# Kernel optimization log

Hardware: AMD Instinct MI355X
Metric: run time of the kernel (lower is better)

Reference implementation:

```python
import jax, jax.numpy as jnp
import numpy as np

N = 100000   # nodes
E = 1200000  # edges
D = 64       # input_features == hidden_features
L = 3        # num_layers
EPS = 1e-5   # BatchNorm1d eps
SLOPE = 0.2  # LeakyReLU negative slope


def setup_inputs() -> dict:
    key = jax.random.key(0)
    k_x, k_e, k_w = jax.random.split(key, 3)
    x = jax.random.normal(k_x, (N, D), dtype=jnp.float32)
    edge_index = jax.random.randint(k_e, (2, E), 0, N, dtype=jnp.int32)
    # Glorot-ish linear weights per layer, stacked [L, D, D]; bias zeros.
    Ws = jax.random.normal(k_w, (L, D, D), dtype=jnp.float32) / np.float32(np.sqrt(D))
    bs = jnp.zeros((L, D), dtype=jnp.float32)
    # BatchNorm affine params (training-mode batch statistics are used).
    gammas = jnp.ones((L, D), dtype=jnp.float32)
    betas = jnp.zeros((L, D), dtype=jnp.float32)
    return {"x": x, "edge_index": edge_index, "Ws": Ws, "bs": bs,
            "gammas": gammas, "betas": betas}


def reference(x, edge_index, Ws, bs, gammas, betas):
    src, dst = edge_index[0], edge_index[1]
    # GCN symmetric normalization with self-loops: deg = in-degree + 1
    deg = jax.ops.segment_sum(jnp.ones((E,), x.dtype), dst, num_segments=N) + 1.0
    dinv = jax.lax.rsqrt(deg)
    enorm = (dinv[src] * dinv[dst])[:, None]  # [E,1] edge norm
    snorm = (dinv * dinv)[:, None]            # [N,1] self-loop norm
    for l in range(L):
        xw = x @ Ws[l]                                        # [N,D]
        agg = (jax.ops.segment_sum(xw[src] * enorm, dst, num_segments=N)
               + xw * snorm + bs[l])                          # GCNConv output
        h = jnp.where(agg > 0, agg, SLOPE * agg)              # LeakyReLU(0.2)
        mu = h.mean(axis=0)
        var = h.var(axis=0)                                   # biased var (PyTorch BN)
        x = gammas[l] * (h - mu) * jax.lax.rsqrt(var + EPS) + betas[l]
    return x
```

## Files before the change

### kernel.cpp

```cpp
#include <hip/hip_runtime.h>

#define D 64
#define SLOPE 0.2f
#define BN_EPS 1e-5f
#define BSHIFT 9
#define BUCKET 512
#define CHUNK 8192
#define CAP 7168
#define COLCAP (CAP + 7 * BUCKET)

static __device__ __forceinline__ unsigned pk_bf16(float fx, float fy) {
    unsigned bx = __float_as_uint(fx);
    unsigned by = __float_as_uint(fy);
    bx = (bx + 0x7fffu + ((bx >> 16) & 1u)) >> 16;
    by = (by + 0x7fffu + ((by >> 16) & 1u)) & 0xffff0000u;
    return bx | by;
}
static __device__ __forceinline__ float bf_lo(unsigned u) { return __uint_as_float(u << 16); }
static __device__ __forceinline__ float bf_hi(unsigned u) { return __uint_as_float(u & 0xffff0000u); }

__global__ __launch_bounds__(256) void k_part(const int* __restrict__ src,
                                              const int* __restrict__ dst,
                                              int* __restrict__ pcur,
                                              unsigned* __restrict__ arena, int E) {
    __shared__ unsigned stage[CHUNK];
    __shared__ unsigned char bktb[CHUNK];
    __shared__ int hist[256], lofs[256], gbase[256];
    const int t = threadIdx.x;
    const int e0 = blockIdx.x * CHUNK;
    const int cn = min(CHUNK, E - e0);

    hist[t] = 0;
    __syncthreads();
    for (int i = t; i < cn; i += 256)
        atomicAdd(&hist[dst[e0 + i] >> BSHIFT], 1);
    __syncthreads();
    const int v = hist[t];
    lofs[t] = v;
    __syncthreads();
    for (int off = 1; off < 256; off <<= 1) {
        int x = lofs[t];
        if (t >= off) x += lofs[t - off];
        __syncthreads();
        lofs[t] = x;
        __syncthreads();
    }
    const int excl = lofs[t] - v;
    __syncthreads();
    lofs[t] = excl;
    if (v > 0) gbase[t] = t * CAP + atomicAdd(&pcur[t], v);
    __syncthreads();
    for (int i = t; i < cn; i += 256) {
        const int dd = dst[e0 + i];
        const int b  = dd >> BSHIFT;
        const int p  = atomicAdd(&lofs[b], 1);
        stage[p] = ((unsigned)(dd & (BUCKET - 1)) << 23) | (unsigned)src[e0 + i];
        bktb[p]  = (unsigned char)b;
    }
    __syncthreads();
    for (int i = t; i < cn; i += 256) {
        const int b = bktb[i];
        const int startb = lofs[b] - hist[b];
        arena[gbase[b] + (i - startb)] = stage[i];
    }
}

__global__ __launch_bounds__(512) void k_build(const unsigned* __restrict__ arena,
                                               const int* __restrict__ pcur,
                                               int* __restrict__ rp, int* __restrict__ pcnt,
                                               int* __restrict__ colbuf, float* __restrict__ dinv,
                                               unsigned* __restrict__ ybf, int N, int HS) {
    __shared__ int ncnt[512], sc[512], lcur[512];
    const int t = threadIdx.x;
    const int b = blockIdx.x;
    const int nbase  = b << BSHIFT;
    const int nlocal = min(BUCKET, N - nbase);
    const int count  = pcur[b];
    const unsigned* ab = arena + (size_t)b * CAP;
    const int colbase = b * COLCAP;

    if (b == 0 && t < 32)
        ybf[(size_t)(t >> 4) * HS + (size_t)N * 16 + (t & 15)] = 0u;

    ncnt[t] = 0;
    __syncthreads();
    for (int i = t; i < count; i += 512)
        atomicAdd(&ncnt[ab[i] >> 23], 1);
    __syncthreads();
    const int v = ncnt[t];
    const int p = (v + 7) & ~7;
    sc[t] = p;
    __syncthreads();
    for (int off = 1; off < 512; off <<= 1) {
        int x = sc[t];
        if (t >= off) x += sc[t - off];
        __syncthreads();
        sc[t] = x;
        __syncthreads();
    }
    const int excl = sc[t] - p;
    lcur[t] = colbase + excl;
    if (t < nlocal) {
        rp[nbase + t]   = colbase + excl;
        pcnt[nbase + t] = p;
        dinv[nbase + t] = rsqrtf((float)v + 1.0f);
    }
    __syncthreads();
    for (int i = t; i < count; i += 512) {
        const unsigned u = ab[i];
        const int pos = atomicAdd(&lcur[u >> 23], 1);
        colbuf[pos] = (int)(u & 0x7FFFFFu);
    }
    if (t < nlocal)
        for (int k = v; k < p; ++k) colbuf[colbase + excl + k] = N;
}

__global__ __launch_bounds__(256) void k_gemm(const float* __restrict__ x,
                                              const float* __restrict__ W,
                                              const float* __restrict__ stats,
                                              const float* __restrict__ gamma,
                                              const float* __restrict__ beta,
                                              const float* __restrict__ dinv,
                                              unsigned* __restrict__ ybf,
                                              float invN, int affine, int N, int HS) {
    __shared__ float scs[D], shs[D];
    const int tid = threadIdx.x;
    if (tid < D) {
        float sc = 1.f, sh = 0.f;
        if (affine) {
            const float mu  = stats[tid] * invN;
            const float var = stats[D + tid] * invN - mu * mu;
            sc = gamma[tid] * rsqrtf(var + BN_EPS);
            sh = beta[tid] - mu * sc;
        }
        scs[tid] = sc; shs[tid] = sh;
    }
    __syncthreads();
    const int lane = tid & 63;
    const int wib  = tid >> 6;
    const int half = lane >> 5;
    const int sl16 = (lane >> 1) & 15;
    float Wreg[D];
    float bv = 0.f;
#pragma unroll
    for (int k = 0; k < D; ++k) {
        const float w = W[k * D + lane];
        Wreg[k] = scs[k] * w;
        bv = fmaf(shs[k], w, bv);
    }
    const int stride = gridDim.x * 4;
    for (int row = __builtin_amdgcn_readfirstlane(blockIdx.x * 4 + wib); row < N; row += stride) {
        const float4* xr = (const float4*)(x + (size_t)row * D);
        float acc = 0.f;
#pragma unroll
        for (int k4 = 0; k4 < 16; ++k4) {
            const float4 xv = xr[k4];
            acc = fmaf(xv.x, Wreg[4 * k4 + 0], acc);
            acc = fmaf(xv.y, Wreg[4 * k4 + 1], acc);
            acc = fmaf(xv.z, Wreg[4 * k4 + 2], acc);
            acc = fmaf(xv.w, Wreg[4 * k4 + 3], acc);
        }
        const float r  = (acc + bv) * dinv[row];
        const float rn = __shfl_down(r, 1, 64);
        if (!(lane & 1))
            ybf[(size_t)half * HS + (size_t)row * 16 + sl16] = pk_bf16(r, rn);
    }
}

__global__ __launch_bounds__(256) void k_pull(const int* __restrict__ rp,
                                              const int* __restrict__ pcnt,
                                              const int* __restrict__ colbuf,
                                              const unsigned* __restrict__ ybf,
                                              const float* __restrict__ dinv,
                                              const float* __restrict__ b,
                                              float* __restrict__ h,
                                              float* __restrict__ stats, int N, int HS) {
    const int tid  = threadIdx.x;
    const int lane = tid & 63;
    const int t16  = lane & 15;
    const int qw   = lane >> 4;
    const int wv   = tid >> 6;
    const int gw   = blockIdx.x * 4 + wv;
    const int gstride = gridDim.x * 4;

    float s1[2][2] = {{0.f, 0.f}, {0.f, 0.f}};
    float s2[2][2] = {{0.f, 0.f}, {0.f, 0.f}};

#pragma unroll
    for (int half = 0; half < 2; ++half) {
        const unsigned* yb = ybf + (size_t)half * HS;
        const float b0 = b[half * 32 + 2 * t16];
        const float b1 = b[half * 32 + 2 * t16 + 1];

        for (int pr = gw; 4 * pr < N; pr += gstride) {
            const int n  = 4 * pr + qw;
            const bool vn = n < N;
            const int st = vn ? rp[n]   : 0;
            const int pd = vn ? pcnt[n] : 0;

            float a[8][2];
#pragma unroll
            for (int c = 0; c < 8; ++c) { a[c][0] = 0.f; a[c][1] = 0.f; }
            {
                const unsigned u = vn ? yb[(size_t)n * 16 + t16] : 0u;
                a[0][0] = bf_lo(u); a[0][1] = bf_hi(u);
            }
            for (int w0 = 0; w0 < pd; w0 += 16) {
                const int wn = min(pd - w0, 16);
                const int ci = (t16 < wn) ? colbuf[st + w0 + t16] : 0;
                for (int j0 = 0; j0 < wn; j0 += 8) {
#pragma unroll
                    for (int jj = 0; jj < 8; ++jj) {
                        const int idx = __shfl(ci, qw * 16 + j0 + jj, 64);
                        const unsigned u = yb[(size_t)idx * 16 + t16];
                        a[jj][0] += bf_lo(u);
                        a[jj][1] += bf_hi(u);
                    }
                }
            }
            const float v0 = ((a[0][0] + a[1][0]) + (a[2][0] + a[3][0])) +
                             ((a[4][0] + a[5][0]) + (a[6][0] + a[7][0]));
            const float v1 = ((a[0][1] + a[1][1]) + (a[2][1] + a[3][1])) +
                             ((a[4][1] + a[5][1]) + (a[6][1] + a[7][1]));
            if (vn) {
                const float di = dinv[n];
                float t0 = fmaf(di, v0, b0); t0 = t0 > 0.f ? t0 : SLOPE * t0;
                float t1 = fmaf(di, v1, b1); t1 = t1 > 0.f ? t1 : SLOPE * t1;
                *(float2*)&h[(size_t)n * D + half * 32 + 2 * t16] = make_float2(t0, t1);
                s1[half][0] += t0; s2[half][0] += t0 * t0;
                s1[half][1] += t1; s2[half][1] += t1 * t1;
            }
        }
    }

    __shared__ float l1[64], l2[64];
    if (tid < 64) { l1[tid] = 0.f; l2[tid] = 0.f; }
    __syncthreads();
#pragma unroll
    for (int half = 0; half < 2; ++half) {
        atomicAdd(&l1[half * 32 + 2 * t16],     s1[half][0]);
        atomicAdd(&l1[half * 32 + 2 * t16 + 1], s1[half][1]);
        atomicAdd(&l2[half * 32 + 2 * t16],     s2[half][0]);
        atomicAdd(&l2[half * 32 + 2 * t16 + 1], s2[half][1]);
    }
    __syncthreads();
    if (tid < 64) {
        atomicAdd(&stats[tid],      l1[tid]);
        atomicAdd(&stats[64 + tid], l2[tid]);
    }
}

__global__ __launch_bounds__(256) void k_normalize(const float* __restrict__ h,
                                                   const float* __restrict__ stats,
                                                   const float* __restrict__ gamma,
                                                   const float* __restrict__ beta,
                                                   float* __restrict__ out,
                                                   float invN, int total4) {
    const int gt = blockIdx.x * 256 + threadIdx.x;
    const int c0 = (gt * 4) & 63;
    float sc[4], sh[4];
#pragma unroll
    for (int k = 0; k < 4; ++k) {
        const int c = c0 + k;
        const float mu  = stats[c] * invN;
        const float var = stats[64 + c] * invN - mu * mu;
        sc[k] = gamma[c] * rsqrtf(var + BN_EPS);
        sh[k] = beta[c] - mu * sc[k];
    }
    const float4* h4 = (const float4*)h;
    float4* o4 = (float4*)out;
    for (int i = gt; i < total4; i += gridDim.x * 256) {
        float4 v = h4[i];
        v.x = fmaf(sc[0], v.x, sh[0]);
        v.y = fmaf(sc[1], v.y, sh[1]);
        v.z = fmaf(sc[2], v.z, sh[2]);
        v.w = fmaf(sc[3], v.w, sh[3]);
        o4[i] = v;
    }
}

extern "C" void kernel_launch(void* const* d_in, const int* in_sizes, int n_in,
                              void* d_out, int out_size, void* d_ws, size_t ws_size,
                              hipStream_t stream) {
    const float* x0     = (const float*)d_in[0];
    const int*   ei     = (const int*)d_in[1];
    const float* Ws     = (const float*)d_in[2];
    const float* bs     = (const float*)d_in[3];
    const float* gammas = (const float*)d_in[4];
    const float* betas  = (const float*)d_in[5];

    const int N = in_sizes[0] / D;
    const int E = in_sizes[1] / 2;
    const int L = in_sizes[2] / (D * D);
    const int nchunks = (E + CHUNK - 1) / CHUNK;
    const int NB = (N + BUCKET - 1) >> BSHIFT;
    const int HS = (N + 1) * 16;

    const int* srcp = ei;
    const int* dstp = ei + E;

    char* wsb = (char*)d_ws;
    size_t o = 0;
    auto alloc = [&](size_t elems) { size_t r = o; o += (elems + 255) & ~(size_t)255; return r; };
    const size_t o_pcur  = alloc(256);
    const size_t o_stats = alloc((size_t)L * 128);
    const size_t zero_end = o;
    const size_t o_rp    = alloc((size_t)N);
    const size_t o_pcnt  = alloc((size_t)N);
    const size_t o_dinv  = alloc((size_t)N);
    const size_t o_arena = alloc((size_t)NB * CAP);
    const size_t o_col   = alloc((size_t)NB * COLCAP);
    const size_t o_y     = alloc((size_t)2 * HS);

    int*      pcur  = (int*)(wsb + o_pcur * 4);
    float*    stats = (float*)(wsb + o_stats * 4);
    int*      rp    = (int*)(wsb + o_rp * 4);
    int*      pcnt  = (int*)(wsb + o_pcnt * 4);
    float*    dinv  = (float*)(wsb + o_dinv * 4);
    unsigned* arena = (unsigned*)(wsb + o_arena * 4);
    int*      col   = (int*)(wsb + o_col * 4);
    unsigned* ybf   = (unsigned*)(wsb + o_y * 4);
    float*    out   = (float*)d_out;
    float*    h     = out;

    hipMemsetAsync(d_ws, 0, zero_end * 4, stream);

    k_part <<<nchunks, 256, 0, stream>>>(srcp, dstp, pcur, arena, E);
    k_build<<<NB, 512, 0, stream>>>(arena, pcur, rp, pcnt, col, dinv, ybf, N, HS);

    const float invN = 1.0f / (float)N;
    const float* xin = x0;
    for (int l = 0; l < L; ++l) {
        const int pl = l ? l - 1 : 0;
        k_gemm<<<1024, 256, 0, stream>>>(xin, Ws + (size_t)l * D * D,
                                         stats + (size_t)pl * 128,
                                         gammas + (size_t)pl * D, betas + (size_t)pl * D,
                                         dinv, ybf, invN, l > 0 ? 1 : 0, N, HS);
        k_pull<<<2048, 256, 0, stream>>>(rp, pcnt, col, ybf, dinv,
                                         bs + (size_t)l * D, h,
                                         stats + (size_t)l * 128, N, HS);
        xin = h;
    }
    k_normalize<<<1024, 256, 0, stream>>>(h, stats + (size_t)(L - 1) * 128,
                                          gammas + (size_t)(L - 1) * D,
                                          betas + (size_t)(L - 1) * D,
                                          out, invN, N * D / 4);
}
```

Baseline: 442.5 us.

## Store bf16 features as full 128-byte rows and gather in one pass

Replaces the split layout, where each node's 64 bf16 features sat in two separate 64-byte half-planes gathered in two passes, with a single interleaved layout of 128 bytes per node. The pull kernel now handles two nodes per wavefront with 32 lanes each and gathers every neighbor row once, which halves the colbuf index reads and loop passes. The cost is a larger per-row gather footprint, which may reduce L2 hit locality compared with the half-plane scheme. Per-lane degree imbalance now spans two nodes instead of four.

```diff
diff --git a/kernel.cpp b/kernel.cpp
--- a/kernel.cpp
+++ b/kernel.cpp
@@ -69,7 +69,7 @@
                                                const int* __restrict__ pcur,
                                                int* __restrict__ rp, int* __restrict__ pcnt,
                                                int* __restrict__ colbuf, float* __restrict__ dinv,
-                                               unsigned* __restrict__ ybf, int N, int HS) {
+                                               unsigned* __restrict__ ybf, int N) {
     __shared__ int ncnt[512], sc[512], lcur[512];
     const int t = threadIdx.x;
     const int b = blockIdx.x;
@@ -79,8 +79,7 @@
     const unsigned* ab = arena + (size_t)b * CAP;
     const int colbase = b * COLCAP;
 
-    if (b == 0 && t < 32)
-        ybf[(size_t)(t >> 4) * HS + (size_t)N * 16 + (t & 15)] = 0u;
+    if (b == 0 && t < 32) ybf[(size_t)N * 32 + t] = 0u;
 
     ncnt[t] = 0;
     __syncthreads();
@@ -122,7 +121,7 @@
                                               const float* __restrict__ beta,
                                               const float* __restrict__ dinv,
                                               unsigned* __restrict__ ybf,
-                                              float invN, int affine, int N, int HS) {
+                                              float invN, int affine, int N) {
     __shared__ float scs[D], shs[D];
     const int tid = threadIdx.x;
     if (tid < D) {
@@ -138,8 +137,6 @@
     __syncthreads();
     const int lane = tid & 63;
     const int wib  = tid >> 6;
-    const int half = lane >> 5;
-    const int sl16 = (lane >> 1) & 15;
     float Wreg[D];
     float bv = 0.f;
 #pragma unroll
@@ -163,7 +160,7 @@
         const float r  = (acc + bv) * dinv[row];
         const float rn = __shfl_down(r, 1, 64);
         if (!(lane & 1))
-            ybf[(size_t)half * HS + (size_t)row * 16 + sl16] = pk_bf16(r, rn);
+            ybf[(size_t)row * 32 + (lane >> 1)] = pk_bf16(r, rn);
     }
 }
 
@@ -174,75 +171,65 @@
                                               const float* __restrict__ dinv,
                                               const float* __restrict__ b,
                                               float* __restrict__ h,
-                                              float* __restrict__ stats, int N, int HS) {
+                                              float* __restrict__ stats, int N) {
     const int tid  = threadIdx.x;
     const int lane = tid & 63;
-    const int t16  = lane & 15;
-    const int qw   = lane >> 4;
+    const int t32  = lane & 31;
+    const int hw   = lane >> 5;
     const int wv   = tid >> 6;
-    const int gw   = blockIdx.x * 4 + wv;
+    const float b0 = b[2 * t32];
+    const float b1 = b[2 * t32 + 1];
+    float s1a = 0.f, s1b = 0.f, s2a = 0.f, s2b = 0.f;
+    const int gw = blockIdx.x * 4 + wv;
     const int gstride = gridDim.x * 4;
 
-    float s1[2][2] = {{0.f, 0.f}, {0.f, 0.f}};
-    float s2[2][2] = {{0.f, 0.f}, {0.f, 0.f}};
-
-#pragma unroll
-    for (int half = 0; half < 2; ++half) {
-        const unsigned* yb = ybf + (size_t)half * HS;
-        const float b0 = b[half * 32 + 2 * t16];
-        const float b1 = b[half * 32 + 2 * t16 + 1];
-
-        for (int pr = gw; 4 * pr < N; pr += gstride) {
-            const int n  = 4 * pr + qw;
-            const bool vn = n < N;
-            const int st = vn ? rp[n]   : 0;
-            const int pd = vn ? pcnt[n] : 0;
-
-            float a[8][2];
-#pragma unroll
-            for (int c = 0; c < 8; ++c) { a[c][0] = 0.f; a[c][1] = 0.f; }
-            {
-                const unsigned u = vn ? yb[(size_t)n * 16 + t16] : 0u;
-                a[0][0] = bf_lo(u); a[0][1] = bf_hi(u);
-            }
-            for (int w0 = 0; w0 < pd; w0 += 16) {
-                const int wn = min(pd - w0, 16);
-                const int ci = (t16 < wn) ? colbuf[st + w0 + t16] : 0;
-                for (int j0 = 0; j0 < wn; j0 += 8) {
-#pragma unroll
-                    for (int jj = 0; jj < 8; ++jj) {
-                        const int idx = __shfl(ci, qw * 16 + j0 + jj, 64);
-                        const unsigned u = yb[(size_t)idx * 16 + t16];
-                        a[jj][0] += bf_lo(u);
-                        a[jj][1] += bf_hi(u);
-                    }
+    for (int pr = gw; 2 * pr < N; pr += gstride) {
+        const int n  = 2 * pr + hw;
+        const bool vn = n < N;
+        const int st = vn ? rp[n]   : 0;
+        const int pd = vn ? pcnt[n] : 0;
+
+        float a[8][2];
+#pragma unroll
+        for (int c = 0; c < 8; ++c) { a[c][0] = 0.f; a[c][1] = 0.f; }
+        {
+            const unsigned u = vn ? ybf[(size_t)n * 32 + t32] : 0u;
+            a[0][0] = bf_lo(u); a[0][1] = bf_hi(u);
+        }
+        for (int w0 = 0; w0 < pd; w0 += 32) {
+            const int wn = min(pd - w0, 32);
+            const int ci = (t32 < wn) ? colbuf[st + w0 + t32] : 0;
+            for (int j0 = 0; j0 < wn; j0 += 8) {
+#pragma unroll
+                for (int jj = 0; jj < 8; ++jj) {
+                    const int idx = __shfl(ci, hw * 32 + j0 + jj, 64);
+                    const unsigned u = ybf[(size_t)idx * 32 + t32];
+                    a[jj][0] += bf_lo(u);
+                    a[jj][1] += bf_hi(u);
                 }
             }
-            const float v0 = ((a[0][0] + a[1][0]) + (a[2][0] + a[3][0])) +
-                             ((a[4][0] + a[5][0]) + (a[6][0] + a[7][0]));
-            const float v1 = ((a[0][1] + a[1][1]) + (a[2][1] + a[3][1])) +
-                             ((a[4][1] + a[5][1]) + (a[6][1] + a[7][1]));
-            if (vn) {
-                const float di = dinv[n];
-                float t0 = fmaf(di, v0, b0); t0 = t0 > 0.f ? t0 : SLOPE * t0;
-                float t1 = fmaf(di, v1, b1); t1 = t1 > 0.f ? t1 : SLOPE * t1;
-                *(float2*)&h[(size_t)n * D + half * 32 + 2 * t16] = make_float2(t0, t1);
-                s1[half][0] += t0; s2[half][0] += t0 * t0;
-                s1[half][1] += t1; s2[half][1] += t1 * t1;
-            }
+        }
+        const float v0 = ((a[0][0] + a[1][0]) + (a[2][0] + a[3][0])) +
+                         ((a[4][0] + a[5][0]) + (a[6][0] + a[7][0]));
+        const float v1 = ((a[0][1] + a[1][1]) + (a[2][1] + a[3][1])) +
+                         ((a[4][1] + a[5][1]) + (a[6][1] + a[7][1]));
+        if (vn) {
+            const float di = dinv[n];
+            float t0 = fmaf(di, v0, b0); t0 = t0 > 0.f ? t0 : SLOPE * t0;
+            float t1 = fmaf(di, v1, b1); t1 = t1 > 0.f ? t1 : SLOPE * t1;
+            *(float2*)&h[(size_t)n * D + 2 * t32] = make_float2(t0, t1);
+            s1a += t0; s2a += t0 * t0;
+            s1b += t1; s2b += t1 * t1;
         }
     }
 
     __shared__ float l1[64], l2[64];
     if (tid < 64) { l1[tid] = 0.f; l2[tid] = 0.f; }
     __syncthreads();
-#pragma unroll
-    for (int half = 0; half < 2; ++half) {
-        atomicAdd(&l1[half * 32 + 2 * t16],     s1[half][0]);
-        atomicAdd(&l1[half * 32 + 2 * t16 + 1], s1[half][1]);
-        atomicAdd(&l2[half * 32 + 2 * t16],     s2[half][0]);
-        atomicAdd(&l2[half * 32 + 2 * t16 + 1], s2[half][1]);
-    }
+    atomicAdd(&l1[2 * t32],     s1a);
+    atomicAdd(&l1[2 * t32 + 1], s1b);
+    atomicAdd(&l2[2 * t32],     s2a);
+    atomicAdd(&l2[2 * t32 + 1], s2b);
     __syncthreads();
     if (tid < 64) {
         atomicAdd(&stats[tid],      l1[tid]);
@@ -294,7 +281,6 @@
     const int L = in_sizes[2] / (D * D);
     const int nchunks = (E + CHUNK - 1) / CHUNK;
     const int NB = (N + BUCKET - 1) >> BSHIFT;
-    const int HS = (N + 1) * 16;
 
     const int* srcp = ei;
     const int* dstp = ei + E;
@@ -310,7 +296,7 @@
     const size_t o_dinv  = alloc((size_t)N);
     const size_t o_arena = alloc((size_t)NB * CAP);
     const size_t o_col   = alloc((size_t)NB * COLCAP);
-    const size_t o_y     = alloc((size_t)2 * HS);
+    const size_t o_y     = alloc(((size_t)N + 1) * 32);
 
     int*      pcur  = (int*)(wsb + o_pcur * 4);
     float*    stats = (float*)(wsb + o_stats * 4);
@@ -326,7 +312,7 @@
     hipMemsetAsync(d_ws, 0, zero_end * 4, stream);
 
     k_part <<<nchunks, 256, 0, stream>>>(srcp, dstp, pcur, arena, E);
-    k_build<<<NB, 512, 0, stream>>>(arena, pcur, rp, pcnt, col, dinv, ybf, N, HS);
+    k_build<<<NB, 512, 0, stream>>>(arena, pcur, rp, pcnt, col, dinv, ybf, N);
 
     const float invN = 1.0f / (float)N;
     const float* xin = x0;
@@ -335,10 +321,10 @@
         k_gemm<<<1024, 256, 0, stream>>>(xin, Ws + (size_t)l * D * D,
                                          stats + (size_t)pl * 128,
                                          gammas + (size_t)pl * D, betas + (size_t)pl * D,
-                                         dinv, ybf, invN, l > 0 ? 1 : 0, N, HS);
+                                         dinv, ybf, invN, l > 0 ? 1 : 0, N);
         k_pull<<<2048, 256, 0, stream>>>(rp, pcnt, col, ybf, dinv,
                                          bs + (size_t)l * D, h,
-                                         stats + (size_t)l * 128, N, HS);
+                                         stats + (size_t)l * 128, N);
         xin = h;
     }
     k_normalize<<<1024, 256, 0, stream>>>(h, stats + (size_t)(L - 1) * 128,
```

Result: faster. 391.4 us (median of 2 runs) (-11.6%).
